# Performance work log

Hardware: AMD Instinct MI355X
Metric: run time of the kernel (lower is better)

## Reference

```python
import jax, jax.numpy as jnp
import numpy as np

NEG = -jnp.inf


def _pipeline(logits, presence_penalties, frequency_penalties, repetition_penalties,
              temperatures, top_p, min_p, top_a, tfs, typical_p,
              epsilon_cutoff, eta_cutoff, smoothing_factor, smoothing_curve,
              prompt_tokens, output_tokens, top_k):
    N, V = logits.shape
    rows = jnp.arange(N)[:, None]
    cols = jnp.arange(V)[None, :]

    # ---- presence / frequency / repetition penalties (bincount via scatter-add) ----
    pbin = jnp.zeros((N, V + 1), jnp.int32).at[rows, prompt_tokens].add(1)[:, :V]
    obin = jnp.zeros((N, V + 1), jnp.int32).at[rows, output_tokens].add(1)[:, :V]
    seen = (pbin > 0) | (obin > 0)
    rp = jnp.where(seen, repetition_penalties[:, None], 1.0)
    logits = jnp.where(logits > 0, logits / rp, logits * rp)
    logits = logits - frequency_penalties[:, None] * obin.astype(logits.dtype)
    logits = logits - presence_penalties[:, None] * (obin > 0).astype(logits.dtype)

    # ---- temperature ----
    logits = logits / temperatures[:, None]

    # ---- top-k + top-p (sort ascending, mask, unsort) ----
    order = jnp.argsort(logits, axis=-1)               # ascending
    ls = jnp.take_along_axis(logits, order, axis=-1)
    kth_pos = (V - jnp.clip(top_k.astype(jnp.int32), 1, V))[:, None]
    kth_val = jnp.take_along_axis(ls, kth_pos, axis=1)
    ls = jnp.where(ls < kth_val, NEG, ls)
    cs = jnp.cumsum(jax.nn.softmax(ls, axis=-1), axis=-1)
    pmask = (cs <= (1.0 - top_p)[:, None]).at[:, -1].set(False)
    ls = jnp.where(pmask, NEG, ls)
    logits = jnp.take_along_axis(ls, jnp.argsort(order, axis=-1), axis=-1)

    # ---- tail-free sampling (sort descending, 2nd-derivative CDF cutoff) ----
    order_d = jnp.argsort(-logits, axis=-1)            # descending order of logits
    ls = jnp.take_along_axis(logits, order_d, axis=-1)
    probs = jax.nn.softmax(ls, axis=-1)
    d2 = jnp.abs(jnp.diff(jnp.diff(probs, axis=-1), axis=-1))   # (N, V-2)
    cdf = jnp.cumsum(d2 / jnp.sum(d2, axis=-1, keepdims=True), axis=-1)
    m = cdf > tfs[:, None]
    m = jnp.concatenate([jnp.zeros((N, 1), bool), m, jnp.ones((N, 1), bool)], axis=-1)
    ls = jnp.where(m, NEG, ls)
    logits = jnp.take_along_axis(ls, jnp.argsort(order_d, axis=-1), axis=-1)

    # ---- eta cutoff (entropy-adaptive threshold, always keep argmax) ----
    sl = jax.nn.log_softmax(logits, axis=-1)
    probs = jnp.exp(sl)
    sl_safe = jnp.where(probs > 0, sl, 0.0)            # nansum equivalent
    neg_ent = jnp.sum(probs * sl_safe, axis=-1)
    eps = jnp.minimum(eta_cutoff, jnp.sqrt(eta_cutoff) * jnp.exp(neg_ent))[:, None]
    top_idx = jnp.argmax(probs, axis=-1)[:, None]
    logits = jnp.where((probs < eps) & (cols != top_idx), NEG, logits)

    # ---- epsilon cutoff (absolute prob threshold, always keep argmax) ----
    probs = jax.nn.softmax(logits, axis=-1)
    top_idx = jnp.argmax(probs, axis=-1)[:, None]
    logits = jnp.where((probs < epsilon_cutoff[:, None]) & (cols != top_idx), NEG, logits)

    # ---- locally typical sampling ----
    sl = jax.nn.log_softmax(logits, axis=-1)
    probs = jnp.exp(sl)
    sl_safe = jnp.where(probs > 0, sl, 0.0)
    neg_ent = jnp.sum(probs * sl_safe, axis=-1, keepdims=True)
    dev = jnp.abs(neg_ent - sl)                        # surprisal deviation
    order_t = jnp.argsort(dev, axis=-1)
    rp2 = jnp.take_along_axis(probs, order_t, axis=-1)
    msort = (jnp.cumsum(rp2, axis=-1) >= typical_p[:, None]).at[:, 0].set(False)
    mask = jnp.zeros((N, V), bool).at[rows, order_t].set(msort)
    logits = jnp.where(mask, NEG, logits)

    # ---- quadratic (smoothing) sampling ----
    mx = jnp.max(logits, axis=-1, keepdims=True)
    finite = logits != NEG
    diff = jnp.where(finite, logits, mx) - mx          # finite everywhere
    kq = (3.0 - smoothing_curve[:, None]) / 2.0
    sq = (smoothing_curve[:, None] - 1.0) / 2.0
    sfc = smoothing_factor[:, None]
    trans = -(kq * sfc * diff ** 2) + sq * sfc * diff ** 3 + mx
    trans = jnp.where(finite, trans, logits)
    logits = jnp.where(sfc > 0, trans, logits)

    # ---- min-p ----
    probs = jax.nn.softmax(logits, axis=-1)
    top_prob = jnp.max(probs, axis=-1, keepdims=True)
    logits = jnp.where(probs < min_p[:, None] * top_prob, NEG, logits)

    # ---- top-a ----
    probs = jax.nn.softmax(logits, axis=-1)
    top_prob = jnp.max(probs, axis=-1, keepdims=True)
    logits = jnp.where(probs < top_a[:, None] * top_prob ** 2, NEG, logits)

    return logits


def setup_inputs() -> dict:
    N, V, PL, OL = 256, 50257, 512, 128
    ks = jax.random.split(jax.random.key(0), 17)
    u = lambda k, lo, hi: lo + (hi - lo) * jax.random.uniform(k, (N,), jnp.float32)
    return {
        "logits": 3.0 * jax.random.normal(ks[0], (N, V), jnp.float32),
        "prompt_tokens": jax.random.randint(ks[1], (N, PL), 0, V),
        "output_tokens": jax.random.randint(ks[2], (N, OL), 0, V),
        "presence_penalties": u(ks[3], 0.0, 0.5),
        "frequency_penalties": u(ks[4], 0.0, 0.5),
        "repetition_penalties": u(ks[5], 1.0, 1.3),
        "temperatures": u(ks[6], 0.5, 1.5),
        "top_p": u(ks[7], 0.85, 0.99),
        "top_k": jax.random.randint(ks[8], (N,), 1, 2048, dtype=jnp.int32),
        "min_p": u(ks[9], 0.0, 0.05),
        "top_a": u(ks[10], 0.0, 0.1),
        "tfs": u(ks[11], 0.95, 0.999),
        "typical_p": u(ks[12], 0.9, 0.999),
        "epsilon_cutoff": u(ks[13], 1e-5, 1e-4),
        "eta_cutoff": u(ks[14], 1e-5, 1e-4),
        "smoothing_factor": u(ks[15], 0.05, 0.25),
        "smoothing_curve": u(ks[16], 1.0, 2.0),
    }


def reference(logits, prompt_tokens, output_tokens, presence_penalties,
              frequency_penalties, repetition_penalties, temperatures, top_p,
              top_k, min_p, top_a, tfs, typical_p, epsilon_cutoff, eta_cutoff,
              smoothing_factor, smoothing_curve):
    return _pipeline(logits, presence_penalties, frequency_penalties,
                     repetition_penalties, temperatures, top_p, min_p, top_a,
                     tfs, typical_p, epsilon_cutoff, eta_cutoff,
                     smoothing_factor, smoothing_curve,
                     prompt_tokens, output_tokens, top_k)
```

## Files before the change

kernel.cpp:

```cpp
#include <hip/hip_runtime.h>
#include <stdint.h>

#define TPB 1024
#define NWAVE 16
#define MAXK 2304
#define NV4 13
#define BIG_NEG (-1.0e30f)

__device__ __forceinline__ uint32_t fkey(float x) {
  uint32_t s = __float_as_uint(x);
  return (s & 0x80000000u) ? ~s : (s | 0x80000000u);
}
__device__ __forceinline__ float fkey_inv(uint32_t u) {
  uint32_t s = (u & 0x80000000u) ? (u & 0x7fffffffu) : ~u;
  return __uint_as_float(s);
}
__device__ __forceinline__ unsigned long long shfl_xor_u64(unsigned long long v, int m) {
  uint32_t lo = (uint32_t)v, hi = (uint32_t)(v >> 32);
  lo = (uint32_t)__shfl_xor((int)lo, m, 64);
  hi = (uint32_t)__shfl_xor((int)hi, m, 64);
  return (((unsigned long long)hi) << 32) | lo;
}

struct TokMem { uint32_t obin[12568]; uint32_t seen[1600]; };
struct SortMem { unsigned long long kp[4096]; };
union U1 { TokMem tok; SortMem srt; };

__device__ __forceinline__ float block_sum1(float v, float* buf) {
  int lane = threadIdx.x & 63, wd = threadIdx.x >> 6;
#pragma unroll
  for (int off = 32; off > 0; off >>= 1) v += __shfl_down(v, off, 64);
  if (lane == 0) buf[wd] = v;
  __syncthreads();
  float r = 0.f;
#pragma unroll
  for (int i = 0; i < NWAVE; i++) r += buf[i];
  return r;
}
__device__ __forceinline__ int block_count(int c, float* buf) {
  return (int)block_sum1((float)c, buf);
}

__device__ void block_scan3(float* arr, int m, float* wbuf) {
  int tid = (int)threadIdx.x, lane = tid & 63, wd = tid >> 6;
  int b = tid * 3;
  __syncthreads();
  float a0 = (b < m) ? arr[b] : 0.f;
  float a1 = (b + 1 < m) ? arr[b + 1] : 0.f;
  float a2 = (b + 2 < m) ? arr[b + 2] : 0.f;
  float c1 = a0 + a1, c2 = c1 + a2;
  float t = c2, w = c2;
#pragma unroll
  for (int off = 1; off < 64; off <<= 1) {
    float x = __shfl_up(w, off, 64);
    if (lane >= off) w += x;
  }
  if (lane == 63) wbuf[wd] = w;
  __syncthreads();
  float base = 0.f;
  for (int i = 0; i < wd; ++i) base += wbuf[i];
  float excl = base + (w - t);
  if (b < m) arr[b] = a0 + excl;
  if (b + 1 < m) arr[b + 1] = c1 + excl;
  if (b + 2 < m) arr[b + 2] = c2 + excl;
  __syncthreads();
}

__device__ void block_scan3x2(float* A, float* B, int m, float* wbufA, float* wbufB) {
  int tid = (int)threadIdx.x, lane = tid & 63, wd = tid >> 6;
  int b = tid * 3;
  __syncthreads();
  float a0 = (b < m) ? A[b] : 0.f;
  float a1 = (b + 1 < m) ? A[b + 1] : 0.f;
  float a2 = (b + 2 < m) ? A[b + 2] : 0.f;
  float x0 = (b < m) ? B[b] : 0.f;
  float x1 = (b + 1 < m) ? B[b + 1] : 0.f;
  float x2 = (b + 2 < m) ? B[b + 2] : 0.f;
  float ca1 = a0 + a1, ca2 = ca1 + a2;
  float cx1 = x0 + x1, cx2 = cx1 + x2;
  float ta = ca2, wa = ca2, tx = cx2, wx = cx2;
#pragma unroll
  for (int off = 1; off < 64; off <<= 1) {
    float sa = __shfl_up(wa, off, 64);
    float sx = __shfl_up(wx, off, 64);
    if (lane >= off) { wa += sa; wx += sx; }
  }
  if (lane == 63) { wbufA[wd] = wa; wbufB[wd] = wx; }
  __syncthreads();
  float baseA = 0.f, baseB = 0.f;
  for (int i = 0; i < wd; ++i) { baseA += wbufA[i]; baseB += wbufB[i]; }
  float exA = baseA + (wa - ta), exB = baseB + (wx - tx);
  if (b < m) { A[b] = a0 + exA; B[b] = x0 + exB; }
  if (b + 1 < m) { A[b + 1] = ca1 + exA; B[b + 1] = cx1 + exB; }
  if (b + 2 < m) { A[b + 2] = ca2 + exA; B[b + 2] = cx2 + exB; }
  __syncthreads();
}

__device__ uint32_t wave_select_digit(const uint32_t (*hist)[256], uint32_t* w_io) {
  int lane = threadIdx.x & 63;
  uint32_t w = *w_io;
  uint32_t c0 = 0, c1 = 0, c2 = 0, c3 = 0;
#pragma unroll
  for (int rp = 0; rp < NWAVE; ++rp) {
    c0 += hist[rp][4 * lane + 0];
    c1 += hist[rp][4 * lane + 1];
    c2 += hist[rp][4 * lane + 2];
    c3 += hist[rp][4 * lane + 3];
  }
  uint32_t t0 = c0 + c1 + c2 + c3;
  uint32_t W = t0;
#pragma unroll
  for (int off = 1; off < 64; off <<= 1) {
    uint32_t x = (uint32_t)__shfl_down((int)W, off, 64);
    if (lane + off < 64) W += x;
  }
  uint32_t Wn = (uint32_t)__shfl_down((int)W, 1, 64);
  if (lane == 63) Wn = 0;
  uint32_t S0 = W, S1 = W - c0, S2 = S1 - c1, S3 = S2 - c2, S4 = Wn;
  int dloc = -1; uint32_t wloc = 0;
  if (S0 >= w && S1 < w) { dloc = 4 * lane + 0; wloc = w - S1; }
  if (S1 >= w && S2 < w) { dloc = 4 * lane + 1; wloc = w - S2; }
  if (S2 >= w && S3 < w) { dloc = 4 * lane + 2; wloc = w - S3; }
  if (S3 >= w && S4 < w) { dloc = 4 * lane + 3; wloc = w - S4; }
  unsigned long long bm = __ballot(dloc >= 0);
  int src = (int)__popcll(bm - 1ull);
  uint32_t d = (uint32_t)__shfl(dloc, src, 64);
  *w_io = (uint32_t)__shfl((int)wloc, src, 64);
  return d;
}

__device__ uint32_t wave_select_digit2k(const uint32_t* __restrict__ h, uint32_t* w_io) {
  int lane = threadIdx.x & 63;
  uint32_t w = *w_io;
  const int base = lane << 5;
  uint32_t lsum = 0;
#pragma unroll
  for (int t = 0; t < 8; ++t) {
    const int tt = (t + lane) & 7;
    const uint4 v = *(const uint4*)(h + base + tt * 4);
    lsum += v.x + v.y + v.z + v.w;
  }
  uint32_t W = lsum;
#pragma unroll
  for (int off = 1; off < 64; off <<= 1) {
    uint32_t x = (uint32_t)__shfl_down((int)W, off, 64);
    if (lane + off < 64) W += x;
  }
  uint32_t Wn = (uint32_t)__shfl_down((int)W, 1, 64);
  if (lane == 63) Wn = 0;
  const bool isb = (W >= w) && (Wn < w);
  int dloc = -1; uint32_t wloc = 0;
  if (isb) {
    uint32_t sfx = Wn;
#pragma unroll
    for (int t = 31; t >= 0; --t) {
      uint32_t c = h[base + t];
      uint32_t si = sfx + c;
      if (si >= w && sfx < w) { dloc = base + t; wloc = w - sfx; }
      sfx = si;
    }
  }
  unsigned long long bm = __ballot(dloc >= 0);
  int src = (int)__popcll(bm - 1ull);
  uint32_t d = (uint32_t)__shfl(dloc, src, 64);
  *w_io = (uint32_t)__shfl((int)wloc, src, 64);
  return d;
}

template <int NE, bool PING>
__device__ void hybrid_sort(unsigned long long* kp, unsigned long long* kb1, int n) {
  const int tid = (int)threadIdx.x;
  unsigned long long k[NE];
#pragma unroll
  for (int e = 0; e < NE; ++e) {
    int i = e * TPB + tid;
    k[e] = (i < n) ? kp[i] : ~0ull;
  }
  int pb = 0;
  for (int kk = 2; kk <= n; kk <<= 1) {
    for (int j = kk >> 1; j > 0; j >>= 1) {
      if (j >= TPB) {
        const int em = j / TPB;
#pragma unroll
        for (int e = 0; e < NE; ++e) {
          if ((e & em) == 0 && (e + em) < NE) {
            int e2 = e + em;
            int i = e * TPB + tid;
            bool up = ((i & kk) == 0);
            if ((k[e] > k[e2]) == up) {
              unsigned long long tk = k[e]; k[e] = k[e2]; k[e2] = tk;
            }
          }
        }
      } else if (j >= 64) {
        unsigned long long* kb = (PING && pb) ? kb1 : kp;
#pragma unroll
        for (int e = 0; e < NE; ++e) {
          int i = e * TPB + tid;
          if (i < n) kb[i] = k[e];
        }
        __syncthreads();
#pragma unroll
        for (int e = 0; e < NE; ++e) {
          int i = e * TPB + tid;
          if (i < n) {
            unsigned long long o = kb[i ^ j];
            bool up = ((i & kk) == 0);
            bool lower = ((i & j) == 0);
            bool takeMin = (lower == up);
            bool takeOther = takeMin ? (o < k[e]) : (o > k[e]);
            if (takeOther) k[e] = o;
          }
        }
        if (PING) pb ^= 1;
        else __syncthreads();
      } else {
#pragma unroll
        for (int e = 0; e < NE; ++e) {
          int i = e * TPB + tid;
          unsigned long long o = shfl_xor_u64(k[e], j);
          bool up = ((i & kk) == 0);
          bool lower = ((i & j) == 0);
          bool takeMin = (lower == up);
          bool takeOther = takeMin ? (o < k[e]) : (o > k[e]);
          if (takeOther) k[e] = o;
        }
      }
    }
  }
  __syncthreads();
#pragma unroll
  for (int e = 0; e < NE; ++e) {
    int i = e * TPB + tid;
    if (i < n) kp[i] = k[e];
  }
  __syncthreads();
}

__device__ __forceinline__ uint32_t penal_key(float l, int j,
    const uint32_t* __restrict__ seen, const uint32_t* __restrict__ obin,
    float f_rep, float inv_rep, float f_freq, float f_pres, float inv_temp) {
  bool sn = (seen[j >> 5] >> (j & 31)) & 1u;
  int ob = 0;
  if (sn) ob = (int)((obin[j >> 2] >> (8 * (j & 3))) & 255u);
  l = (l > 0.0f) ? (l * (sn ? inv_rep : 1.0f)) : (l * (sn ? f_rep : 1.0f));
  l = l - f_freq * (float)ob;
  l = l - ((ob > 0) ? f_pres : 0.0f);
  l = l * inv_temp;
  return fkey(l);
}

#define FOR_ELEMS(...) do {                                                   \
    if (tid < head) { int j = tid; uint32_t u = uh; (void)j; (void)u; __VA_ARGS__; } \
    _Pragma("unroll")                                                         \
    for (int s4_ = 0; s4_ < NV4; ++s4_) {                                     \
      int iv_ = s4_ * TPB + tid;                                              \
      if (iv_ < nvec) {                                                       \
        int jb_ = head + 4 * iv_;                                             \
        { int j = jb_ + 0; uint32_t u = uk[s4_ * 4 + 0]; (void)j; (void)u; __VA_ARGS__; } \
        { int j = jb_ + 1; uint32_t u = uk[s4_ * 4 + 1]; (void)j; (void)u; __VA_ARGS__; } \
        { int j = jb_ + 2; uint32_t u = uk[s4_ * 4 + 2]; (void)j; (void)u; __VA_ARGS__; } \
        { int j = jb_ + 3; uint32_t u = uk[s4_ * 4 + 3]; (void)j; (void)u; __VA_ARGS__; } \
      }                                                                       \
    }                                                                         \
    if (tid < ntail) { int j = head + 4 * nvec + tid; uint32_t u = ut; (void)j; (void)u; __VA_ARGS__; } \
  } while (0)

#define COLLECT_ELEM do {                                                     \
    bool pk_ = (u >= kth_u);                                                  \
    unsigned long long bm_ = __ballot(pk_);                                   \
    if (bm_) {                                                                \
      uint32_t base_ = 0;                                                     \
      if (lane == 0) base_ = atomicAdd(&s_cnt, (uint32_t)__popcll(bm_));      \
      base_ = (uint32_t)__shfl((int)base_, 0, 64);                            \
      if (pk_) {                                                              \
        uint32_t pos_ = base_ + (uint32_t)__popcll(bm_ & ((1ull << (unsigned)lane) - 1ull)); \
        if (pos_ < MAXK)                                                      \
          kp[pos_] = (((unsigned long long)(~u)) << 16) | (unsigned long long)(uint32_t)j; \
      }                                                                       \
    }                                                                         \
  } while (0)

__global__ __launch_bounds__(TPB, 4)
void sampler_kernel(const float* __restrict__ logits,
                    const int* __restrict__ ptoks, const int* __restrict__ otoks,
                    const float* __restrict__ pres, const float* __restrict__ freq,
                    const float* __restrict__ rep, const float* __restrict__ temp,
                    const float* __restrict__ topp, const int* __restrict__ topk,
                    const float* __restrict__ minp, const float* __restrict__ topa,
                    const float* __restrict__ tfsv, const float* __restrict__ typp,
                    const float* __restrict__ epsc, const float* __restrict__ etac,
                    const float* __restrict__ smf, const float* __restrict__ smc,
                    float* __restrict__ out, int N, int V, int PL, int OL) {
  __shared__ U1 u1;
  __shared__ uint32_t s_hist[NWAVE][256];
  __shared__ uint32_t s_hist2k[2048];
  __shared__ float s_e[MAXK];
  __shared__ float s_p[MAXK];
  __shared__ float s_q[MAXK];
  __shared__ float s_r[MAXK];
  __shared__ unsigned long long kb1[2048];
  __shared__ float s_site[12][NWAVE];
  __shared__ uint32_t s_cnt;

  const int tid = (int)threadIdx.x;
  const int r = (int)blockIdx.x;
  const int wd = tid >> 6;
  const int lane = tid & 63;

  const float* lrow = logits + (size_t)r * V;
  float* orow = out + (size_t)r * V;

  for (int i = tid; i < 12568; i += TPB) u1.tok.obin[i] = 0;
  for (int i = tid; i < 1600; i += TPB) u1.tok.seen[i] = 0;
  for (int i = lane; i < 256; i += 64) s_hist[wd][i] = 0;
  for (int i = tid; i < 2048; i += TPB) s_hist2k[i] = 0;
  if (tid == 0) s_cnt = 0;
  __syncthreads();
  for (int i = tid; i < PL; i += TPB) {
    int t = ptoks[(size_t)r * PL + i];
    if ((unsigned)t < (unsigned)V) atomicOr(&u1.tok.seen[t >> 5], 1u << (t & 31));
  }
  for (int i = tid; i < OL; i += TPB) {
    int t = otoks[(size_t)r * OL + i];
    if ((unsigned)t < (unsigned)V) {
      atomicOr(&u1.tok.seen[t >> 5], 1u << (t & 31));
      atomicAdd(&u1.tok.obin[t >> 2], 1u << (8 * (t & 3)));
    }
  }
  __syncthreads();

  const float f_pres = pres[r], f_freq = freq[r], f_rep = rep[r], f_temp = temp[r];
  const float f_topp = topp[r], f_minp = minp[r], f_topa = topa[r], f_tfs = tfsv[r];
  const float f_typp = typp[r], f_epsc = epsc[r], f_etac = etac[r];
  const float f_smf = smf[r], f_smc = smc[r];
  const float inv_rep = 1.0f / f_rep, inv_temp = 1.0f / f_temp;
  int k_topk = topk[r];
  if (k_topk < 1) k_topk = 1;
  if (k_topk > V) k_topk = V;

  const uint32_t* seenp = u1.tok.seen;
  const uint32_t* obinp = u1.tok.obin;

  uintptr_t ra = (uintptr_t)lrow;
  int head = (int)(((16u - (uint32_t)(ra & 15u)) & 15u) >> 2);
  if (head > V) head = V;
  const int nvec = (V - head) >> 2;
  const int ntail = V - head - (nvec << 2);

  uint32_t uk[NV4 * 4];
  uint32_t uh = 0, ut = 0;
#pragma unroll
  for (int s4 = 0; s4 < NV4; ++s4) {
    int iv = s4 * TPB + tid;
    uint32_t u0 = 0, u1k = 0, u2k = 0, u3 = 0;
    if (iv < nvec) {
      const float4 lv = *(const float4*)(lrow + head + 4 * iv);
      int jb = head + 4 * iv;
      u0 = penal_key(lv.x, jb + 0, seenp, obinp, f_rep, inv_rep, f_freq, f_pres, inv_temp);
      u1k = penal_key(lv.y, jb + 1, seenp, obinp, f_rep, inv_rep, f_freq, f_pres, inv_temp);
      u2k = penal_key(lv.z, jb + 2, seenp, obinp, f_rep, inv_rep, f_freq, f_pres, inv_temp);
      u3 = penal_key(lv.w, jb + 3, seenp, obinp, f_rep, inv_rep, f_freq, f_pres, inv_temp);
      uint32_t b0 = u0 >> 24, b1 = u1k >> 24, b2 = u2k >> 24, b3 = u3 >> 24;
      if (b0 == b1 && b0 == b2 && b0 == b3) {
        atomicAdd(&s_hist[wd][b0], 4u);
      } else {
        atomicAdd(&s_hist[wd][b0], 1u);
        atomicAdd(&s_hist[wd][b1], 1u);
        atomicAdd(&s_hist[wd][b2], 1u);
        atomicAdd(&s_hist[wd][b3], 1u);
      }
    }
    uk[s4 * 4 + 0] = u0; uk[s4 * 4 + 1] = u1k; uk[s4 * 4 + 2] = u2k; uk[s4 * 4 + 3] = u3;
  }
  if (tid < head) {
    uh = penal_key(lrow[tid], tid, seenp, obinp, f_rep, inv_rep, f_freq, f_pres, inv_temp);
    atomicAdd(&s_hist[wd][uh >> 24], 1u);
  }
  if (tid < ntail) {
    int j = head + 4 * nvec + tid;
    ut = penal_key(lrow[j], j, seenp, obinp, f_rep, inv_rep, f_freq, f_pres, inv_temp);
    atomicAdd(&s_hist[wd][ut >> 24], 1u);
  }

  {
    uintptr_t oa = (uintptr_t)orow;
    int ohead = (int)(((16u - (uint32_t)(oa & 15u)) & 15u) >> 2);
    if (ohead > V) ohead = V;
    int onvec = (V - ohead) >> 2;
    for (int j = tid; j < ohead; j += TPB) orow[j] = BIG_NEG;
    float4* o4 = (float4*)(orow + ohead);
    const float4 f4 = make_float4(BIG_NEG, BIG_NEG, BIG_NEG, BIG_NEG);
    for (int i = tid; i < onvec; i += TPB) o4[i] = f4;
    for (int j = ohead + (onvec << 2) + tid; j < V; j += TPB) orow[j] = BIG_NEG;
  }
  __syncthreads();

  uint32_t w = (uint32_t)k_topk;
  uint32_t d3 = wave_select_digit(s_hist, &w);
  FOR_ELEMS(if ((u >> 24) == d3) atomicAdd(&s_hist2k[(u >> 13) & 2047u], 1u));
  __syncthreads();
  uint32_t d11 = wave_select_digit2k(s_hist2k, &w);
  const uint32_t kth_u = (d3 << 24) | (d11 << 13);

  unsigned long long* kp = u1.srt.kp;
  FOR_ELEMS(COLLECT_ELEM);
  __syncthreads();
  int K = (int)s_cnt;
  if (K > MAXK) K = MAXK;

  {
    int n1 = 64; while (n1 < K) n1 <<= 1;
    for (int i = K + tid; i < n1; i += TPB) kp[i] = ~0ull;
    __syncthreads();
    if (n1 <= 1024) hybrid_sort<1, true>(kp, kb1, n1);
    else if (n1 == 2048) hybrid_sort<2, true>(kp, kb1, n1);
    else hybrid_sort<4, false>(kp, nullptr, n1);
  }

  {
    const uint32_t kth_inv = (uint32_t)(kp[k_topk - 1] >> 16);
    int c = 0;
    for (int i = tid; i < K; i += TPB)
      if ((uint32_t)(kp[i] >> 16) <= kth_inv) c++;
    K = block_count(c, s_site[10]);
  }

  const float m0 = fkey_inv(~(uint32_t)(kp[0] >> 16));

  for (int i = tid; i < K; i += TPB) {
    float v = fkey_inv(~(uint32_t)(kp[i] >> 16));
    float e = __expf(v - m0);
    s_e[i] = e; s_p[i] = e; s_q[i] = e * (v - m0);
  }
  block_scan3x2(s_p, s_q, K, s_site[8], s_site[9]);
  const float S = s_p[K - 1];

  {
    const float thS = (1.0f - f_topp) * S;
    int c = 0;
    for (int i = tid; i < K; i += TPB) {
      float ss = S - s_p[i] + s_e[i];
      if (i == 0 || ss > thS) c++;
    }
    K = block_count(c, s_site[0]);
  }

  {
    for (int i = tid; i < K; i += TPB) {
      float e0 = s_e[i];
      float e1 = (i + 1 < K) ? s_e[i + 1] : 0.f;
      float e2 = (i + 2 < K) ? s_e[i + 2] : 0.f;
      s_r[i] = fabsf((e2 - e1) - (e1 - e0));
    }
    block_scan3(s_r, K, s_site[7]);
    const float thT = f_tfs * s_r[K - 1];
    int c = 0;
    for (int i = tid; i < K; i += TPB)
      if (i == 0 || s_r[i - 1] <= thT) c++;
    K = block_count(c, s_site[1]);
  }

  {
    const float SD = s_p[K - 1];
    const float ne = s_q[K - 1] / SD - __logf(SD);
    const float eps = fminf(f_etac, sqrtf(f_etac) * __expf(ne));
    const float thD = eps * SD;
    int c = 0;
    for (int i = tid; i < K; i += TPB)
      if (i == 0 || s_e[i] >= thD) c++;
    K = block_count(c, s_site[2]);
  }

  {
    const float thE = f_epsc * s_p[K - 1];
    int c = 0;
    for (int i = tid; i < K; i += TPB)
      if (i == 0 || s_e[i] >= thE) c++;
    K = block_count(c, s_site[3]);
  }

  int i_lo = 0, i_hi = K - 1;
  {
    const float SF = s_p[K - 1];
    const float lseF = __logf(SF);
    const float ne = s_q[K - 1] / SF - lseF;
    const float vth = ne + lseF + m0;
    const float typSF = f_typp * SF;
    int cc = 0;
    for (int i = tid; i < K; i += TPB)
      if (fkey_inv(~(uint32_t)(kp[i] >> 16)) >= vth) cc++;
    const int c = block_count(cc, s_site[4]);
    const int nB = K - c;

    auto keyAt = [&](int i) -> unsigned long long {
      unsigned long long kk = kp[i];
      float v = fkey_inv(~(uint32_t)(kk >> 16));
      return (((unsigned long long)fkey(fabsf(v - vth))) << 16) | (kk & 0xffffull);
    };
    auto splitFor = [&](int p) -> int {
      int alo = p - nB; if (alo < 0) alo = 0;
      int ahi = (p < c) ? p : c;
      while (alo < ahi) {
        int am = (alo + ahi + 1) >> 1;
        int tb = p - am;
        bool take = true;
        if (tb < nB) take = (keyAt(c - am) <= keyAt(c + tb));
        if (take) alo = am; else ahi = am - 1;
      }
      return alo;
    };

    int cnt = 0;
    for (int p = 1 + tid; p <= K; p += TPB) {
      int a = splitFor(p);
      int b = p - a;
      float sum = s_p[c + b - 1] - ((c - a > 0) ? s_p[c - a - 1] : 0.f);
      if (sum < typSF) cnt++;
    }
    int L = block_count(cnt, s_site[5]);
    if (L < 1) L = 1;
    if (L > K) L = K;
    int a = splitFor(L);
    i_lo = c - a;
    i_hi = c + (L - a) - 1;
  }

  float S2;
  const float mx = fkey_inv(~(uint32_t)(kp[i_lo] >> 16));
  {
    const float kq = (3.0f - f_smc) * 0.5f;
    const float sq = (f_smc - 1.0f) * 0.5f;
    float pS = 0.f;
    for (int i = i_lo + tid; i <= i_hi; i += TPB) {
      float v = fkey_inv(~(uint32_t)(kp[i] >> 16));
      float d = v - mx;
      float tr = mx - (kq * f_smf) * (d * d) + (sq * f_smf) * ((d * d) * d);
      float v2 = (f_smf > 0.0f) ? tr : v;
      float e = __expf(v2 - mx);
      s_q[i] = e;
      s_r[i] = v2;
      if (e >= f_minp) pS += e;
    }
    S2 = block_sum1(pS, s_site[6]);
  }

  {
    const float thA = f_topa / S2;
    for (int i = i_lo + tid; i <= i_hi; i += TPB) {
      float e = s_q[i];
      if (e >= f_minp && e >= thA) {
        int idx = (int)(kp[i] & 0xffffull);
        orow[idx] = s_r[i];
      }
    }
  }
}

extern "C" void kernel_launch(void* const* d_in, const int* in_sizes, int n_in,
                              void* d_out, int out_size, void* d_ws, size_t ws_size,
                              hipStream_t stream) {
  const float* logits = (const float*)d_in[0];
  const int* ptoks = (const int*)d_in[1];
  const int* otoks = (const int*)d_in[2];
  const float* pres = (const float*)d_in[3];
  const float* freq = (const float*)d_in[4];
  const float* rep  = (const float*)d_in[5];
  const float* temp = (const float*)d_in[6];
  const float* topp = (const float*)d_in[7];
  const int*   topk = (const int*)d_in[8];
  const float* minp = (const float*)d_in[9];
  const float* topa = (const float*)d_in[10];
  const float* tfsv = (const float*)d_in[11];
  const float* typp = (const float*)d_in[12];
  const float* epsc = (const float*)d_in[13];
  const float* etac = (const float*)d_in[14];
  const float* smf  = (const float*)d_in[15];
  const float* smc  = (const float*)d_in[16];

  int N = in_sizes[3];
  int V = in_sizes[0] / N;
  int PL = in_sizes[1] / N;
  int OL = in_sizes[2] / N;

  sampler_kernel<<<N, TPB, 0, stream>>>(logits, ptoks, otoks, pres, freq, rep, temp,
                                        topp, topk, minp, topa, tfsv, typp, epsc, etac,
                                        smf, smc, (float*)d_out, N, V, PL, OL);
}
```

Baseline: 82.43 us.

## Reorder radix select to 11+8 bits and binary-search typical cutoff

Top-k radix select now histograms the top 11 bits first into a single shared 2048-bin histogram, then the next 8 bits into a 256-bin histogram. This replaces the previous 8-then-11 order that used per-wave 256-bin histograms. The typical-p cutoff no longer counts masses across all K positions block-wide; one wave runs a 64-way parallel search over the monotone predicate. Smaller changes vectorize shared-memory zeroing and wave-buffer reductions and load the seen bitmask once per float4. In exchange, atomics all hit one shared histogram, which may raise contention, and only one wave does the search while the others idle.

After: 70.51 us. -14.5%, faster.

```diff
diff --git a/kernel.cpp b/kernel.cpp
--- a/kernel.cpp
+++ b/kernel.cpp
@@ -24,7 +24,7 @@
 
 struct TokMem { uint32_t obin[12568]; uint32_t seen[1600]; };
 struct SortMem { unsigned long long kp[4096]; };
-union U1 { TokMem tok; SortMem srt; };
+union __align__(16) U1 { TokMem tok; SortMem srt; };
 
 __device__ __forceinline__ float block_sum1(float v, float* buf) {
   int lane = threadIdx.x & 63, wd = threadIdx.x >> 6;
@@ -32,13 +32,27 @@
   for (int off = 32; off > 0; off >>= 1) v += __shfl_down(v, off, 64);
   if (lane == 0) buf[wd] = v;
   __syncthreads();
-  float r = 0.f;
-#pragma unroll
-  for (int i = 0; i < NWAVE; i++) r += buf[i];
+  const float4* b4 = (const float4*)buf;
+  float4 A = b4[0], B = b4[1], C = b4[2], D = b4[3];
+  float r = A.x; r += A.y; r += A.z; r += A.w;
+  r += B.x; r += B.y; r += B.z; r += B.w;
+  r += C.x; r += C.y; r += C.z; r += C.w;
+  r += D.x; r += D.y; r += D.z; r += D.w;
   return r;
 }
 __device__ __forceinline__ int block_count(int c, float* buf) {
   return (int)block_sum1((float)c, buf);
+}
+
+__device__ __forceinline__ float wbuf_prefix(const float* wbuf, int wd) {
+  const float4* w4 = (const float4*)wbuf;
+  float4 a = w4[0], b = w4[1], c = w4[2], d = w4[3];
+  float t[16] = {a.x, a.y, a.z, a.w, b.x, b.y, b.z, b.w,
+                 c.x, c.y, c.z, c.w, d.x, d.y, d.z, d.w};
+  float base = 0.f;
+#pragma unroll
+  for (int i = 0; i < 16; ++i) base += (i < wd) ? t[i] : 0.f;
+  return base;
 }
 
 __device__ void block_scan3(float* arr, int m, float* wbuf) {
@@ -57,8 +71,7 @@
   }
   if (lane == 63) wbuf[wd] = w;
   __syncthreads();
-  float base = 0.f;
-  for (int i = 0; i < wd; ++i) base += wbuf[i];
+  float base = wbuf_prefix(wbuf, wd);
   float excl = base + (w - t);
   if (b < m) arr[b] = a0 + excl;
   if (b + 1 < m) arr[b + 1] = c1 + excl;
@@ -87,8 +100,8 @@
   }
   if (lane == 63) { wbufA[wd] = wa; wbufB[wd] = wx; }
   __syncthreads();
-  float baseA = 0.f, baseB = 0.f;
-  for (int i = 0; i < wd; ++i) { baseA += wbufA[i]; baseB += wbufB[i]; }
+  float baseA = wbuf_prefix(wbufA, wd);
+  float baseB = wbuf_prefix(wbufB, wd);
   float exA = baseA + (wa - ta), exB = baseB + (wx - tx);
   if (b < m) { A[b] = a0 + exA; B[b] = x0 + exB; }
   if (b + 1 < m) { A[b + 1] = ca1 + exA; B[b + 1] = cx1 + exB; }
@@ -96,17 +109,49 @@
   __syncthreads();
 }
 
-__device__ uint32_t wave_select_digit(const uint32_t (*hist)[256], uint32_t* w_io) {
+__device__ uint32_t wave_select_digit2k(const uint32_t* __restrict__ h, uint32_t* w_io) {
   int lane = threadIdx.x & 63;
   uint32_t w = *w_io;
-  uint32_t c0 = 0, c1 = 0, c2 = 0, c3 = 0;
-#pragma unroll
-  for (int rp = 0; rp < NWAVE; ++rp) {
-    c0 += hist[rp][4 * lane + 0];
-    c1 += hist[rp][4 * lane + 1];
-    c2 += hist[rp][4 * lane + 2];
-    c3 += hist[rp][4 * lane + 3];
-  }
+  const int base = lane << 5;
+  uint32_t lsum = 0;
+#pragma unroll
+  for (int t = 0; t < 8; ++t) {
+    const int tt = (t + lane) & 7;
+    const uint4 v = *(const uint4*)(h + base + tt * 4);
+    lsum += v.x + v.y + v.z + v.w;
+  }
+  uint32_t W = lsum;
+#pragma unroll
+  for (int off = 1; off < 64; off <<= 1) {
+    uint32_t x = (uint32_t)__shfl_down((int)W, off, 64);
+    if (lane + off < 64) W += x;
+  }
+  uint32_t Wn = (uint32_t)__shfl_down((int)W, 1, 64);
+  if (lane == 63) Wn = 0;
+  const bool isb = (W >= w) && (Wn < w);
+  int dloc = -1; uint32_t wloc = 0;
+  if (isb) {
+    uint32_t sfx = Wn;
+#pragma unroll
+    for (int t = 31; t >= 0; --t) {
+      uint32_t c = h[base + t];
+      uint32_t si = sfx + c;
+      if (si >= w && sfx < w) { dloc = base + t; wloc = w - sfx; }
+      sfx = si;
+    }
+  }
+  unsigned long long bm = __ballot(dloc >= 0);
+  int src = (int)__popcll(bm - 1ull);
+  uint32_t d = (uint32_t)__shfl(dloc, src, 64);
+  *w_io = (uint32_t)__shfl((int)wloc, src, 64);
+  return d;
+}
+
+__device__ uint32_t wave_select_digit256(const uint32_t* __restrict__ h, uint32_t* w_io) {
+  int lane = threadIdx.x & 63;
+  uint32_t w = *w_io;
+  const uint4 v = ((const uint4*)h)[lane];
+  uint32_t c0 = v.x, c1 = v.y, c2 = v.z, c3 = v.w;
   uint32_t t0 = c0 + c1 + c2 + c3;
   uint32_t W = t0;
 #pragma unroll
@@ -122,44 +167,6 @@
   if (S1 >= w && S2 < w) { dloc = 4 * lane + 1; wloc = w - S2; }
   if (S2 >= w && S3 < w) { dloc = 4 * lane + 2; wloc = w - S3; }
   if (S3 >= w && S4 < w) { dloc = 4 * lane + 3; wloc = w - S4; }
-  unsigned long long bm = __ballot(dloc >= 0);
-  int src = (int)__popcll(bm - 1ull);
-  uint32_t d = (uint32_t)__shfl(dloc, src, 64);
-  *w_io = (uint32_t)__shfl((int)wloc, src, 64);
-  return d;
-}
-
-__device__ uint32_t wave_select_digit2k(const uint32_t* __restrict__ h, uint32_t* w_io) {
-  int lane = threadIdx.x & 63;
-  uint32_t w = *w_io;
-  const int base = lane << 5;
-  uint32_t lsum = 0;
-#pragma unroll
-  for (int t = 0; t < 8; ++t) {
-    const int tt = (t + lane) & 7;
-    const uint4 v = *(const uint4*)(h + base + tt * 4);
-    lsum += v.x + v.y + v.z + v.w;
-  }
-  uint32_t W = lsum;
-#pragma unroll
-  for (int off = 1; off < 64; off <<= 1) {
-    uint32_t x = (uint32_t)__shfl_down((int)W, off, 64);
-    if (lane + off < 64) W += x;
-  }
-  uint32_t Wn = (uint32_t)__shfl_down((int)W, 1, 64);
-  if (lane == 63) Wn = 0;
-  const bool isb = (W >= w) && (Wn < w);
-  int dloc = -1; uint32_t wloc = 0;
-  if (isb) {
-    uint32_t sfx = Wn;
-#pragma unroll
-    for (int t = 31; t >= 0; --t) {
-      uint32_t c = h[base + t];
-      uint32_t si = sfx + c;
-      if (si >= w && sfx < w) { dloc = base + t; wloc = w - sfx; }
-      sfx = si;
-    }
-  }
   unsigned long long bm = __ballot(dloc >= 0);
   int src = (int)__popcll(bm - 1ull);
   uint32_t d = (uint32_t)__shfl(dloc, src, 64);
@@ -237,10 +244,9 @@
   __syncthreads();
 }
 
-__device__ __forceinline__ uint32_t penal_key(float l, int j,
-    const uint32_t* __restrict__ seen, const uint32_t* __restrict__ obin,
+__device__ __forceinline__ uint32_t penal_val(float l, int j, bool sn,
+    const uint32_t* __restrict__ obin,
     float f_rep, float inv_rep, float f_freq, float f_pres, float inv_temp) {
-  bool sn = (seen[j >> 5] >> (j & 31)) & 1u;
   int ob = 0;
   if (sn) ob = (int)((obin[j >> 2] >> (8 * (j & 3))) & 255u);
   l = (l > 0.0f) ? (l * (sn ? inv_rep : 1.0f)) : (l * (sn ? f_rep : 1.0f));
@@ -248,6 +254,12 @@
   l = l - ((ob > 0) ? f_pres : 0.0f);
   l = l * inv_temp;
   return fkey(l);
+}
+__device__ __forceinline__ uint32_t penal_key(float l, int j,
+    const uint32_t* __restrict__ seen, const uint32_t* __restrict__ obin,
+    float f_rep, float inv_rep, float f_freq, float f_pres, float inv_temp) {
+  bool sn = (seen[j >> 5] >> (j & 31)) & 1u;
+  return penal_val(l, j, sn, obin, f_rep, inv_rep, f_freq, f_pres, inv_temp);
 }
 
 #define FOR_ELEMS(...) do {                                                   \
@@ -293,15 +305,16 @@
                     const float* __restrict__ smf, const float* __restrict__ smc,
                     float* __restrict__ out, int N, int V, int PL, int OL) {
   __shared__ U1 u1;
-  __shared__ uint32_t s_hist[NWAVE][256];
-  __shared__ uint32_t s_hist2k[2048];
+  __shared__ __align__(16) uint32_t s_hist2k[2048];
+  __shared__ __align__(16) uint32_t s_h256[256];
   __shared__ float s_e[MAXK];
   __shared__ float s_p[MAXK];
   __shared__ float s_q[MAXK];
   __shared__ float s_r[MAXK];
   __shared__ unsigned long long kb1[2048];
-  __shared__ float s_site[12][NWAVE];
+  __shared__ __align__(16) float s_site[12][NWAVE];
   __shared__ uint32_t s_cnt;
+  __shared__ int s_ilo, s_ihi;
 
   const int tid = (int)threadIdx.x;
   const int r = (int)blockIdx.x;
@@ -311,10 +324,16 @@
   const float* lrow = logits + (size_t)r * V;
   float* orow = out + (size_t)r * V;
 
-  for (int i = tid; i < 12568; i += TPB) u1.tok.obin[i] = 0;
-  for (int i = tid; i < 1600; i += TPB) u1.tok.seen[i] = 0;
-  for (int i = lane; i < 256; i += 64) s_hist[wd][i] = 0;
-  for (int i = tid; i < 2048; i += TPB) s_hist2k[i] = 0;
+  {
+    const uint4 z4 = make_uint4(0u, 0u, 0u, 0u);
+    uint4* ob4 = (uint4*)u1.tok.obin;
+    for (int i = tid; i < 3142; i += TPB) ob4[i] = z4;
+    uint4* se4 = (uint4*)u1.tok.seen;
+    for (int i = tid; i < 400; i += TPB) se4[i] = z4;
+    uint4* h4 = (uint4*)s_hist2k;
+    for (int i = tid; i < 512; i += TPB) h4[i] = z4;
+    if (tid < 64) ((uint4*)s_h256)[tid] = z4;
+  }
   if (tid == 0) s_cnt = 0;
   __syncthreads();
   for (int i = tid; i < PL; i += TPB) {
@@ -357,30 +376,28 @@
     if (iv < nvec) {
       const float4 lv = *(const float4*)(lrow + head + 4 * iv);
       int jb = head + 4 * iv;
-      u0 = penal_key(lv.x, jb + 0, seenp, obinp, f_rep, inv_rep, f_freq, f_pres, inv_temp);
-      u1k = penal_key(lv.y, jb + 1, seenp, obinp, f_rep, inv_rep, f_freq, f_pres, inv_temp);
-      u2k = penal_key(lv.z, jb + 2, seenp, obinp, f_rep, inv_rep, f_freq, f_pres, inv_temp);
-      u3 = penal_key(lv.w, jb + 3, seenp, obinp, f_rep, inv_rep, f_freq, f_pres, inv_temp);
-      uint32_t b0 = u0 >> 24, b1 = u1k >> 24, b2 = u2k >> 24, b3 = u3 >> 24;
-      if (b0 == b1 && b0 == b2 && b0 == b3) {
-        atomicAdd(&s_hist[wd][b0], 4u);
-      } else {
-        atomicAdd(&s_hist[wd][b0], 1u);
-        atomicAdd(&s_hist[wd][b1], 1u);
-        atomicAdd(&s_hist[wd][b2], 1u);
-        atomicAdd(&s_hist[wd][b3], 1u);
-      }
+      uint32_t w0 = seenp[jb >> 5];
+      uint32_t w1 = seenp[(jb >> 5) + 1];
+      uint32_t sb = (uint32_t)(((((uint64_t)w1) << 32) | (uint64_t)w0) >> (jb & 31));
+      u0 = penal_val(lv.x, jb + 0, (sb >> 0) & 1u, obinp, f_rep, inv_rep, f_freq, f_pres, inv_temp);
+      u1k = penal_val(lv.y, jb + 1, (sb >> 1) & 1u, obinp, f_rep, inv_rep, f_freq, f_pres, inv_temp);
+      u2k = penal_val(lv.z, jb + 2, (sb >> 2) & 1u, obinp, f_rep, inv_rep, f_freq, f_pres, inv_temp);
+      u3 = penal_val(lv.w, jb + 3, (sb >> 3) & 1u, obinp, f_rep, inv_rep, f_freq, f_pres, inv_temp);
+      atomicAdd(&s_hist2k[u0 >> 21], 1u);
+      atomicAdd(&s_hist2k[u1k >> 21], 1u);
+      atomicAdd(&s_hist2k[u2k >> 21], 1u);
+      atomicAdd(&s_hist2k[u3 >> 21], 1u);
     }
     uk[s4 * 4 + 0] = u0; uk[s4 * 4 + 1] = u1k; uk[s4 * 4 + 2] = u2k; uk[s4 * 4 + 3] = u3;
   }
   if (tid < head) {
     uh = penal_key(lrow[tid], tid, seenp, obinp, f_rep, inv_rep, f_freq, f_pres, inv_temp);
-    atomicAdd(&s_hist[wd][uh >> 24], 1u);
+    atomicAdd(&s_hist2k[uh >> 21], 1u);
   }
   if (tid < ntail) {
     int j = head + 4 * nvec + tid;
     ut = penal_key(lrow[j], j, seenp, obinp, f_rep, inv_rep, f_freq, f_pres, inv_temp);
-    atomicAdd(&s_hist[wd][ut >> 24], 1u);
+    atomicAdd(&s_hist2k[ut >> 21], 1u);
   }
 
   {
@@ -397,11 +414,11 @@
   __syncthreads();
 
   uint32_t w = (uint32_t)k_topk;
-  uint32_t d3 = wave_select_digit(s_hist, &w);
-  FOR_ELEMS(if ((u >> 24) == d3) atomicAdd(&s_hist2k[(u >> 13) & 2047u], 1u));
-  __syncthreads();
   uint32_t d11 = wave_select_digit2k(s_hist2k, &w);
-  const uint32_t kth_u = (d3 << 24) | (d11 << 13);
+  FOR_ELEMS(if ((u >> 21) == d11) atomicAdd(&s_h256[(u >> 13) & 255u], 1u));
+  __syncthreads();
+  uint32_t d8 = wave_select_digit256(s_h256, &w);
+  const uint32_t kth_u = (d11 << 21) | (d8 << 13);
 
   unsigned long long* kp = u1.srt.kp;
   FOR_ELEMS(COLLECT_ELEM);
@@ -493,37 +510,52 @@
     const int c = block_count(cc, s_site[4]);
     const int nB = K - c;
 
-    auto keyAt = [&](int i) -> unsigned long long {
-      unsigned long long kk = kp[i];
-      float v = fkey_inv(~(uint32_t)(kk >> 16));
-      return (((unsigned long long)fkey(fabsf(v - vth))) << 16) | (kk & 0xffffull);
-    };
-    auto splitFor = [&](int p) -> int {
-      int alo = p - nB; if (alo < 0) alo = 0;
-      int ahi = (p < c) ? p : c;
-      while (alo < ahi) {
-        int am = (alo + ahi + 1) >> 1;
-        int tb = p - am;
-        bool take = true;
-        if (tb < nB) take = (keyAt(c - am) <= keyAt(c + tb));
-        if (take) alo = am; else ahi = am - 1;
+    if (wd == 0) {
+      auto keyAt = [&](int i) -> unsigned long long {
+        unsigned long long kk = kp[i];
+        float v = fkey_inv(~(uint32_t)(kk >> 16));
+        return (((unsigned long long)fkey(fabsf(v - vth))) << 16) | (kk & 0xffffull);
+      };
+      auto splitFor = [&](int p) -> int {
+        int alo = p - nB; if (alo < 0) alo = 0;
+        int ahi = (p < c) ? p : c;
+        while (alo < ahi) {
+          int am = (alo + ahi + 1) >> 1;
+          int tb = p - am;
+          bool take = true;
+          if (tb < nB) take = (keyAt(c - am) <= keyAt(c + tb));
+          if (take) alo = am; else ahi = am - 1;
+        }
+        return alo;
+      };
+      auto massLess = [&](int p) -> bool {
+        int a = splitFor(p);
+        int b = p - a;
+        float sum = s_p[c + b - 1] - ((c - a > 0) ? s_p[c - a - 1] : 0.f);
+        return sum < typSF;
+      };
+      int plo = 0, phi = K;
+      while (phi > plo) {
+        int range = phi - plo;
+        int stride = (range + 63) >> 6;
+        int p = plo + stride * (lane + 1);
+        bool q = false;
+        if (p <= phi) q = massLess(p);
+        unsigned long long bm = __ballot(q);
+        int h = bm ? (63 - (int)__clzll(bm)) : -1;
+        int nlo = (h >= 0) ? (plo + stride * (h + 1)) : plo;
+        long long nf = (long long)plo + (long long)stride * (long long)(h + 2);
+        int nhi = (nf <= (long long)phi) ? (int)nf - 1 : phi;
+        plo = nlo; phi = nhi;
       }
-      return alo;
-    };
-
-    int cnt = 0;
-    for (int p = 1 + tid; p <= K; p += TPB) {
-      int a = splitFor(p);
-      int b = p - a;
-      float sum = s_p[c + b - 1] - ((c - a > 0) ? s_p[c - a - 1] : 0.f);
-      if (sum < typSF) cnt++;
-    }
-    int L = block_count(cnt, s_site[5]);
-    if (L < 1) L = 1;
-    if (L > K) L = K;
-    int a = splitFor(L);
-    i_lo = c - a;
-    i_hi = c + (L - a) - 1;
+      int L = plo;
+      if (L < 1) L = 1;
+      if (L > K) L = K;
+      int a = splitFor(L);
+      if (lane == 0) { s_ilo = c - a; s_ihi = c + (L - a) - 1; }
+    }
+    __syncthreads();
+    i_lo = s_ilo; i_hi = s_ihi;
   }
 
   float S2;
```
